# Performance work log

Measured on AMD Instinct MI355X. Metric: run time of the kernel, lower is better.

Reference implementation:

```python
import jax, jax.numpy as jnp
import numpy as np

EMBED_DIM = 128
NUM_HEADS = 16
D_K = EMBED_DIM // NUM_HEADS  # n_wires per head = 8
DEPTH = 1
DIM = 2 ** D_K  # 256 state amplitudes


def _cnot_chain_inverse_perm(d, depth):
    """Inverse permutation of basis states under `depth` rounds of the CNOT ladder
    CNOT(0,1),...,CNOT(d-2,d-1),CNOT(d-1,0). Wire 0 = most significant bit."""
    idx = np.arange(2 ** d)
    shifts = d - 1 - np.arange(d)
    bits = (idx[:, None] >> shifts) & 1  # (2^d, d)
    for _ in range(depth):
        for w in range(d - 1):
            bits[:, w + 1] ^= bits[:, w]
        bits[:, 0] ^= bits[:, d - 1]
    fwd = (bits << shifts).sum(axis=1)  # psi'[fwd[b]] = psi[b]
    inv = np.empty_like(fwd)
    inv[fwd] = idx  # psi'[j] = psi[inv[j]]
    return inv


def _pauliz_signs(d):
    idx = np.arange(2 ** d)
    shifts = d - 1 - np.arange(d)
    bits = (idx[:, None] >> shifts) & 1
    return (1.0 - 2.0 * bits).astype(np.float32)  # (2^d, d)


_INV_PERM = jnp.asarray(_cnot_chain_inverse_perm(D_K, DEPTH))
_SIGNS = jnp.asarray(_pauliz_signs(D_K))


def quantum_head(angles):
    """angles: (..., d) RX rotation angles. Returns PauliZ expectations (..., d).

    Product state amplitudes after per-wire RX from |0..0>: probabilities are
    products of cos^2/sin^2; CNOT ladder is a basis permutation; <Z_w> is a
    signed sum of probabilities."""
    half = angles * 0.5
    c2 = jnp.cos(half) ** 2
    s2 = jnp.sin(half) ** 2
    lead = angles.shape[:-1]
    p = jnp.ones(lead + (1,), angles.dtype)
    for w in range(D_K):  # builds (..., 2^d) probability vector
        pair = jnp.stack([c2[..., w], s2[..., w]], axis=-1)
        p = (p[..., :, None] * pair[..., None, :]).reshape(lead + (-1,))
    p = p[..., _INV_PERM]  # apply CNOT ladder permutation
    return p @ _SIGNS  # (..., d) PauliZ expectations


def setup_inputs() -> dict:
    key = jax.random.key(0)
    ks = jax.random.split(key, 10)
    B, S, E = 8, 512, EMBED_DIM
    sc = 1.0 / np.sqrt(E)
    return {
        "x": jax.random.normal(ks[0], (B, S, E), jnp.float32),
        "Wq": jax.random.normal(ks[1], (E, E), jnp.float32) * sc,
        "bq": jnp.zeros((E,), jnp.float32),
        "Wk": jax.random.normal(ks[2], (E, E), jnp.float32) * sc,
        "bk": jnp.zeros((E,), jnp.float32),
        "Wv": jax.random.normal(ks[3], (E, E), jnp.float32) * sc,
        "bv": jnp.zeros((E,), jnp.float32),
        "Wo": jax.random.normal(ks[4], (E, E), jnp.float32) * sc,
        "bo": jnp.zeros((E,), jnp.float32),
        "theta": jax.random.normal(ks[5], (NUM_HEADS, D_K), jnp.float32),
    }


def reference(x, Wq, bq, Wk, bk, Wv, bv, Wo, bo, theta):
    B, S, E = x.shape
    H, dk = NUM_HEADS, D_K

    def split_heads(y):  # (B,S,E) -> (B,H,S,dk)
        return y.reshape(B, S, H, dk).transpose(0, 2, 1, 3)

    q = split_heads(x @ Wq + bq)
    k = split_heads(x @ Wk + bk)
    v = split_heads(x @ Wv + bv)

    th = theta[None, :, None, :]  # broadcast per-head trainable RX angles
    qh = quantum_head(q + th)
    kh = quantum_head(k + th)
    vh = quantum_head(v + th)

    scores = jnp.einsum("bhsd,bhtd->bhst", qh, kh) / jnp.sqrt(jnp.asarray(dk, x.dtype))
    attn = jax.nn.softmax(scores, axis=-1)
    out = jnp.einsum("bhst,bhtd->bhsd", attn, vh)
    out = out.transpose(0, 2, 1, 3).reshape(B, S, E)
    return out @ Wo + bo
```

## Files before the change

### kernel.cpp

```cpp
#include <hip/hip_runtime.h>
#include <hip/hip_bf16.h>
#include <math.h>

#define BB 8
#define SS 512
#define EE 128
#define HH 16
#define DKK 8

#define FMA4(ACC, S, W) do { (ACC).x += (S)*(W).x; (ACC).y += (S)*(W).y; \
                             (ACC).z += (S)*(W).z; (ACC).w += (S)*(W).w; } while(0)
#define ADD4(A, B) do { (A).x += (B).x; (A).y += (B).y; (A).z += (B).z; (A).w += (B).w; } while(0)
#define DOT4(A, B) ((A).x*(B).x + (A).y*(B).y + (A).z*(B).z + (A).w*(B).w)

__global__ __launch_bounds__(256, 4) void k_qkvq(
    const float* __restrict__ x,
    const float* __restrict__ Wq, const float* __restrict__ bq,
    const float* __restrict__ Wk, const float* __restrict__ bk,
    const float* __restrict__ Wv, const float* __restrict__ bv,
    const float* __restrict__ theta,
    float* __restrict__ qh, float* __restrict__ kh, float* __restrict__ vh)
{
    __shared__ float xs[16][128];
    const int t = threadIdx.x;
    const int m = blockIdx.y;
    const int row0 = blockIdx.x * 16;

    {
        const float4* xv = (const float4*)(x + (size_t)row0 * 128);
        float4* xsv = (float4*)&xs[0][0];
        xsv[t]       = xv[t];
        xsv[t + 256] = xv[t + 256];
    }
    __syncthreads();

    const int cg   = t & 31;
    const int col0 = cg * 4;
    const int rg   = t >> 5;
    const int r0   = rg * 2;

    const float* __restrict__ W  = (m == 0) ? Wq : (m == 1) ? Wk : Wv;
    const float* __restrict__ bb = (m == 0) ? bq : (m == 1) ? bk : bv;
    float* __restrict__ outp     = (m == 0) ? qh : (m == 1) ? kh : vh;

    float4 acc0 = *(const float4*)&bb[col0];
    float4 acc1 = acc0;

    #pragma unroll 4
    for (int k4 = 0; k4 < 32; ++k4) {
        const float4 xa = ((const float4*)xs[r0 + 0])[k4];
        const float4 xb = ((const float4*)xs[r0 + 1])[k4];
        const float4 w0 = *(const float4*)&W[(k4 * 4 + 0) * 128 + col0];
        const float4 w1 = *(const float4*)&W[(k4 * 4 + 1) * 128 + col0];
        const float4 w2 = *(const float4*)&W[(k4 * 4 + 2) * 128 + col0];
        const float4 w3 = *(const float4*)&W[(k4 * 4 + 3) * 128 + col0];
        FMA4(acc0, xa.x, w0); FMA4(acc0, xa.y, w1);
        FMA4(acc0, xa.z, w2); FMA4(acc0, xa.w, w3);
        FMA4(acc1, xb.x, w0); FMA4(acc1, xb.y, w1);
        FMA4(acc1, xb.z, w2); FMA4(acc1, xb.w, w3);
    }

    const float4 th = *(const float4*)&theta[col0];
    const int h    = cg >> 1;
    const int half = cg & 1;

    float4 accs[2] = {acc0, acc1};
    #pragma unroll
    for (int r = 0; r < 2; ++r) {
        float4 c;
        c.x = __cosf(accs[r].x + th.x);
        c.y = __cosf(accs[r].y + th.y);
        c.z = __cosf(accs[r].z + th.z);
        c.w = __cosf(accs[r].w + th.w);
        const float p0 = c.x;
        const float p1 = p0 * c.y;
        const float p2 = p1 * c.z;
        const float p3 = p2 * c.w;
        const float recv = __shfl_xor(p3, 1);
        float4 o;
        if (half == 0) {
            o.x = c.y * c.z * c.w * recv;
            o.y = p1; o.z = p2; o.w = p3;
        } else {
            o.x = recv * p0;
            o.y = recv * p1;
            o.z = recv * p2;
            o.w = recv * p3;
        }
        const int g  = row0 + r0 + r;
        const int b_ = g >> 9;
        const int s  = g & 511;
        *(float4*)&outp[(((size_t)b_ * HH + h) * SS + s) * DKK + half * 4] = o;
    }
}

__global__ __launch_bounds__(512, 2) void k_attn(
    const float* __restrict__ qh, const float* __restrict__ kh,
    const float* __restrict__ vh, float* __restrict__ hid)
{
    __shared__ float4 smem[3072];

    const int t  = threadIdx.x;
    const int L  = t & 63;
    const int wv = t >> 6;
    const int bh = blockIdx.x & 127;
    const int q0 = (blockIdx.x >> 7) * 256;

    {
        const float4* kg = (const float4*)kh + (size_t)bh * 1024;
        const float4* vg = (const float4*)vh + (size_t)bh * 1024;
        smem[t]        = kg[t];
        smem[t + 512]  = kg[t + 512];
        smem[1024 + t] = vg[t];
        smem[1536 + t] = vg[t + 512];
    }

    const float sc = 0.51012091944f;
    float4 qa[4], qb[4];
    {
        const float4* qg = (const float4*)qh + ((size_t)bh * 512 + q0) * 2;
        #pragma unroll
        for (int r = 0; r < 4; ++r) {
            float4 a = qg[(L + 64 * r) * 2];
            float4 b = qg[(L + 64 * r) * 2 + 1];
            a.x *= sc; a.y *= sc; a.z *= sc; a.w *= sc;
            b.x *= sc; b.y *= sc; b.z *= sc; b.w *= sc;
            qa[r] = a; qb[r] = b;
        }
    }
    __syncthreads();

    float4 aA[4], aB[4];
    float  den[4];
    #pragma unroll
    for (int r = 0; r < 4; ++r) {
        aA[r] = make_float4(0.f, 0.f, 0.f, 0.f);
        aB[r] = make_float4(0.f, 0.f, 0.f, 0.f);
        den[r] = 0.f;
    }

    const float4* kbase = smem + wv * 128;
    const float4* vbase = smem + 1024 + wv * 128;

    #pragma unroll 4
    for (int j = 0; j < 64; ++j) {
        const float4 k0 = kbase[2 * j];
        const float4 k1 = kbase[2 * j + 1];
        const float4 v0 = vbase[2 * j];
        const float4 v1 = vbase[2 * j + 1];
        #pragma unroll
        for (int r = 0; r < 4; ++r) {
            const float s = DOT4(qa[r], k0) + DOT4(qb[r], k1);
            const float e = exp2f(s);
            den[r] += e;
            FMA4(aA[r], e, v0);
            FMA4(aB[r], e, v1);
        }
    }
    __syncthreads();

    if (wv < 4) {
        #pragma unroll
        for (int r = 0; r < 4; ++r) {
            const int idx = (wv * 256 + L + 64 * r) * 3;
            smem[idx]     = aA[r];
            smem[idx + 1] = aB[r];
            smem[idx + 2] = make_float4(den[r], 0.f, 0.f, 0.f);
        }
    }
    __syncthreads();
    if (wv >= 4) {
        #pragma unroll
        for (int r = 0; r < 4; ++r) {
            const int idx = ((wv - 4) * 256 + L + 64 * r) * 3;
            float4 pa = smem[idx];
            float4 pb = smem[idx + 1];
            float4 pd = smem[idx + 2];
            ADD4(pa, aA[r]); ADD4(pb, aB[r]); pd.x += den[r];
            smem[idx]     = pa;
            smem[idx + 1] = pb;
            smem[idx + 2] = pd;
        }
    }
    __syncthreads();

    if (t < 256) {
        float4 rA = make_float4(0.f, 0.f, 0.f, 0.f), rB = rA;
        float rd = 0.f;
        #pragma unroll
        for (int s4 = 0; s4 < 4; ++s4) {
            const int idx = (s4 * 256 + t) * 3;
            const float4 a = smem[idx];
            const float4 b = smem[idx + 1];
            ADD4(rA, a); ADD4(rB, b);
            rd += smem[idx + 2].x;
        }
        const float inv = 1.0f / rd;
        rA.x *= inv; rA.y *= inv; rA.z *= inv; rA.w *= inv;
        rB.x *= inv; rB.y *= inv; rB.z *= inv; rB.w *= inv;
        const int b_ = bh >> 4, h = bh & 15;
        float* o = hid + ((size_t)(b_ * 512) + q0 + t) * 128 + h * 8;
        ((float4*)o)[0] = rA;
        ((float4*)o)[1] = rB;
    }
}

__global__ __launch_bounds__(256, 4) void k_out(
    const float* __restrict__ hid, const float* __restrict__ Wo,
    const float* __restrict__ bo, float* __restrict__ out)
{
    __shared__ float hs[16][128];
    const int t = threadIdx.x;
    const int row0 = blockIdx.x * 16;

    {
        const float4* hv = (const float4*)(hid + (size_t)row0 * 128);
        float4* hsv = (float4*)&hs[0][0];
        hsv[t]       = hv[t];
        hsv[t + 256] = hv[t + 256];
    }
    __syncthreads();

    const int cg   = t & 31;
    const int col0 = cg * 4;
    const int rg   = t >> 5;
    const int r0   = rg * 2;

    float4 acc0 = *(const float4*)&bo[col0];
    float4 acc1 = acc0;

    #pragma unroll 4
    for (int k4 = 0; k4 < 32; ++k4) {
        const float4 xa = ((const float4*)hs[r0 + 0])[k4];
        const float4 xb = ((const float4*)hs[r0 + 1])[k4];
        const float4 w0 = *(const float4*)&Wo[(k4 * 4 + 0) * 128 + col0];
        const float4 w1 = *(const float4*)&Wo[(k4 * 4 + 1) * 128 + col0];
        const float4 w2 = *(const float4*)&Wo[(k4 * 4 + 2) * 128 + col0];
        const float4 w3 = *(const float4*)&Wo[(k4 * 4 + 3) * 128 + col0];
        FMA4(acc0, xa.x, w0); FMA4(acc0, xa.y, w1);
        FMA4(acc0, xa.z, w2); FMA4(acc0, xa.w, w3);
        FMA4(acc1, xb.x, w0); FMA4(acc1, xb.y, w1);
        FMA4(acc1, xb.z, w2); FMA4(acc1, xb.w, w3);
    }

    *(float4*)&out[(size_t)(row0 + r0 + 0) * 128 + col0] = acc0;
    *(float4*)&out[(size_t)(row0 + r0 + 1) * 128 + col0] = acc1;
}

extern "C" void kernel_launch(void* const* d_in, const int* in_sizes, int n_in,
                              void* d_out, int out_size, void* d_ws, size_t ws_size,
                              hipStream_t stream)
{
    const float* x     = (const float*)d_in[0];
    const float* Wq    = (const float*)d_in[1];
    const float* bq    = (const float*)d_in[2];
    const float* Wk    = (const float*)d_in[3];
    const float* bk    = (const float*)d_in[4];
    const float* Wv    = (const float*)d_in[5];
    const float* bv    = (const float*)d_in[6];
    const float* Wo    = (const float*)d_in[7];
    const float* bo    = (const float*)d_in[8];
    const float* theta = (const float*)d_in[9];
    float* out = (float*)d_out;

    float* ws  = (float*)d_ws;
    float* qh  = ws;
    float* kh  = ws + 524288;
    float* vh  = ws + 1048576;
    float* hid = ws + 1572864;

    k_qkvq<<<dim3(256, 3), 256, 0, stream>>>(x, Wq, bq, Wk, bk, Wv, bv,
                                             theta, qh, kh, vh);
    k_attn<<<256, 512, 0, stream>>>(qh, kh, vh, hid);
    k_out <<<256, 256, 0, stream>>>(hid, Wo, bo, out);
}
```

Before: 47.76 us.

## Fuse output projection into attention kernel via per-head atomic accumulation

Drops the separate output-projection kernel and the hid workspace round trip. Each attention block now multiplies its per-head 8-wide result by the matching 8 rows of Wo and atomically adds its contribution into the output, which the QKV kernel pre-initialises with the bias. This saves one kernel launch and a global write and read of hid. In exchange it issues many float atomics (16 heads add into each output element), and the summation order becomes nondeterministic. It also lowers the QKV kernel's launch-bounds occupancy hint.

```diff
diff --git a/kernel.cpp b/kernel.cpp
--- a/kernel.cpp
+++ b/kernel.cpp
@@ -13,13 +13,14 @@
 #define ADD4(A, B) do { (A).x += (B).x; (A).y += (B).y; (A).z += (B).z; (A).w += (B).w; } while(0)
 #define DOT4(A, B) ((A).x*(B).x + (A).y*(B).y + (A).z*(B).z + (A).w*(B).w)
 
-__global__ __launch_bounds__(256, 4) void k_qkvq(
+__global__ __launch_bounds__(256, 2) void k_qkvq(
     const float* __restrict__ x,
     const float* __restrict__ Wq, const float* __restrict__ bq,
     const float* __restrict__ Wk, const float* __restrict__ bk,
     const float* __restrict__ Wv, const float* __restrict__ bv,
-    const float* __restrict__ theta,
-    float* __restrict__ qh, float* __restrict__ kh, float* __restrict__ vh)
+    const float* __restrict__ theta, const float* __restrict__ bo,
+    float* __restrict__ qh, float* __restrict__ kh, float* __restrict__ vh,
+    float* __restrict__ out)
 {
     __shared__ float xs[16][128];
     const int t = threadIdx.x;
@@ -92,19 +93,28 @@
         const int s  = g & 511;
         *(float4*)&outp[(((size_t)b_ * HH + h) * SS + s) * DKK + half * 4] = o;
     }
+
+    if (m == 0) {
+        const float4 b0 = *(const float4*)&bo[col0];
+        *(float4*)&out[(size_t)(row0 + r0 + 0) * 128 + col0] = b0;
+        *(float4*)&out[(size_t)(row0 + r0 + 1) * 128 + col0] = b0;
+    }
 }
 
-__global__ __launch_bounds__(512, 2) void k_attn(
+__global__ __launch_bounds__(512, 2) void k_attn_out(
     const float* __restrict__ qh, const float* __restrict__ kh,
-    const float* __restrict__ vh, float* __restrict__ hid)
+    const float* __restrict__ vh, const float* __restrict__ Wo,
+    float* __restrict__ out)
 {
-    __shared__ float4 smem[3072];
+    __shared__ float4 smem[3584];
 
     const int t  = threadIdx.x;
     const int L  = t & 63;
     const int wv = t >> 6;
     const int bh = blockIdx.x & 127;
     const int q0 = (blockIdx.x >> 7) * 256;
+    const int b_ = bh >> 4;
+    const int h  = bh & 15;
 
     {
         const float4* kg = (const float4*)kh + (size_t)bh * 1024;
@@ -198,53 +208,30 @@
         const float inv = 1.0f / rd;
         rA.x *= inv; rA.y *= inv; rA.z *= inv; rA.w *= inv;
         rB.x *= inv; rB.y *= inv; rB.z *= inv; rB.w *= inv;
-        const int b_ = bh >> 4, h = bh & 15;
-        float* o = hid + ((size_t)(b_ * 512) + q0 + t) * 128 + h * 8;
-        ((float4*)o)[0] = rA;
-        ((float4*)o)[1] = rB;
-    }
-}
-
-__global__ __launch_bounds__(256, 4) void k_out(
-    const float* __restrict__ hid, const float* __restrict__ Wo,
-    const float* __restrict__ bo, float* __restrict__ out)
-{
-    __shared__ float hs[16][128];
-    const int t = threadIdx.x;
-    const int row0 = blockIdx.x * 16;
-
-    {
-        const float4* hv = (const float4*)(hid + (size_t)row0 * 128);
-        float4* hsv = (float4*)&hs[0][0];
-        hsv[t]       = hv[t];
-        hsv[t + 256] = hv[t + 256];
-    }
-    __syncthreads();
-
-    const int cg   = t & 31;
-    const int col0 = cg * 4;
-    const int rg   = t >> 5;
-    const int r0   = rg * 2;
-
-    float4 acc0 = *(const float4*)&bo[col0];
-    float4 acc1 = acc0;
-
-    #pragma unroll 4
-    for (int k4 = 0; k4 < 32; ++k4) {
-        const float4 xa = ((const float4*)hs[r0 + 0])[k4];
-        const float4 xb = ((const float4*)hs[r0 + 1])[k4];
-        const float4 w0 = *(const float4*)&Wo[(k4 * 4 + 0) * 128 + col0];
-        const float4 w1 = *(const float4*)&Wo[(k4 * 4 + 1) * 128 + col0];
-        const float4 w2 = *(const float4*)&Wo[(k4 * 4 + 2) * 128 + col0];
-        const float4 w3 = *(const float4*)&Wo[(k4 * 4 + 3) * 128 + col0];
-        FMA4(acc0, xa.x, w0); FMA4(acc0, xa.y, w1);
-        FMA4(acc0, xa.z, w2); FMA4(acc0, xa.w, w3);
-        FMA4(acc1, xb.x, w0); FMA4(acc1, xb.y, w1);
-        FMA4(acc1, xb.z, w2); FMA4(acc1, xb.w, w3);
-    }
-
-    *(float4*)&out[(size_t)(row0 + r0 + 0) * 128 + col0] = acc0;
-    *(float4*)&out[(size_t)(row0 + r0 + 1) * 128 + col0] = acc1;
+        smem[3072 + t * 2]     = rA;
+        smem[3072 + t * 2 + 1] = rB;
+    }
+    __syncthreads();
+
+    {
+        const int col = t & 127;
+        const int rg  = t >> 7;
+        float wo[8];
+        #pragma unroll
+        for (int i = 0; i < 8; ++i)
+            wo[i] = Wo[(h * 8 + i) * 128 + col];
+
+        const float* red = (const float*)(smem + 3072);
+        float* obase = out + ((size_t)(b_ * 512) + q0 + rg * 64) * 128 + col;
+        #pragma unroll 4
+        for (int rr = 0; rr < 64; ++rr) {
+            const float4 r0v = *(const float4*)&red[(rg * 64 + rr) * 8];
+            const float4 r1v = *(const float4*)&red[(rg * 64 + rr) * 8 + 4];
+            const float acc = r0v.x*wo[0] + r0v.y*wo[1] + r0v.z*wo[2] + r0v.w*wo[3]
+                            + r1v.x*wo[4] + r1v.y*wo[5] + r1v.z*wo[6] + r1v.w*wo[7];
+            unsafeAtomicAdd(obase + (size_t)rr * 128, acc);
+        }
+    }
 }
 
 extern "C" void kernel_launch(void* const* d_in, const int* in_sizes, int n_in,
@@ -263,14 +250,12 @@
     const float* theta = (const float*)d_in[9];
     float* out = (float*)d_out;
 
-    float* ws  = (float*)d_ws;
-    float* qh  = ws;
-    float* kh  = ws + 524288;
-    float* vh  = ws + 1048576;
-    float* hid = ws + 1572864;
+    float* ws = (float*)d_ws;
+    float* qh = ws;
+    float* kh = ws + 524288;
+    float* vh = ws + 1048576;
 
     k_qkvq<<<dim3(256, 3), 256, 0, stream>>>(x, Wq, bq, Wk, bk, Wv, bv,
-                                             theta, qh, kh, vh);
-    k_attn<<<256, 512, 0, stream>>>(qh, kh, vh, hid);
-    k_out <<<256, 256, 0, stream>>>(hid, Wo, bo, out);
+                                             theta, bo, qh, kh, vh, out);
+    k_attn_out<<<256, 512, 0, stream>>>(qh, kh, vh, Wo, out);
 }
```

Result: slower. 74.00 us (+54.9%).

## Split each wave's key range across half-waves with 8 query rows per lane

Applied to the files above, without the earlier changes.

Each wave previously walked its 64 keys with every lane holding 4 query rows. Now the two half-waves each take half of the wave's keys while every lane holds 8 query rows, and the halves are combined with cross-lane shuffles before the existing shared-memory reduction. This halves LDS reads of K/V per unit of work and exposes more independent exp/FMA chains, at the cost of roughly double the accumulator registers. The occupancy hint in launch bounds is dropped accordingly.

```diff
diff --git a/kernel.cpp b/kernel.cpp
--- a/kernel.cpp
+++ b/kernel.cpp
@@ -94,7 +94,7 @@
     }
 }
 
-__global__ __launch_bounds__(512, 2) void k_attn(
+__global__ __launch_bounds__(512) void k_attn(
     const float* __restrict__ qh, const float* __restrict__ kh,
     const float* __restrict__ vh, float* __restrict__ hid)
 {
@@ -103,6 +103,8 @@
     const int t  = threadIdx.x;
     const int L  = t & 63;
     const int wv = t >> 6;
+    const int hw = L >> 5;
+    const int l5 = L & 31;
     const int bh = blockIdx.x & 127;
     const int q0 = (blockIdx.x >> 7) * 256;
 
@@ -116,13 +118,13 @@
     }
 
     const float sc = 0.51012091944f;
-    float4 qa[4], qb[4];
+    float4 qa[8], qb[8];
     {
         const float4* qg = (const float4*)qh + ((size_t)bh * 512 + q0) * 2;
         #pragma unroll
-        for (int r = 0; r < 4; ++r) {
-            float4 a = qg[(L + 64 * r) * 2];
-            float4 b = qg[(L + 64 * r) * 2 + 1];
+        for (int r = 0; r < 8; ++r) {
+            float4 a = qg[(l5 + 32 * r) * 2];
+            float4 b = qg[(l5 + 32 * r) * 2 + 1];
             a.x *= sc; a.y *= sc; a.z *= sc; a.w *= sc;
             b.x *= sc; b.y *= sc; b.z *= sc; b.w *= sc;
             qa[r] = a; qb[r] = b;
@@ -130,26 +132,26 @@
     }
     __syncthreads();
 
-    float4 aA[4], aB[4];
-    float  den[4];
+    float4 aA[8], aB[8];
+    float  den[8];
     #pragma unroll
-    for (int r = 0; r < 4; ++r) {
+    for (int r = 0; r < 8; ++r) {
         aA[r] = make_float4(0.f, 0.f, 0.f, 0.f);
         aB[r] = make_float4(0.f, 0.f, 0.f, 0.f);
         den[r] = 0.f;
     }
 
-    const float4* kbase = smem + wv * 128;
-    const float4* vbase = smem + 1024 + wv * 128;
+    const float4* kbase = smem + wv * 128 + hw * 64;
+    const float4* vbase = smem + 1024 + wv * 128 + hw * 64;
 
     #pragma unroll 4
-    for (int j = 0; j < 64; ++j) {
-        const float4 k0 = kbase[2 * j];
-        const float4 k1 = kbase[2 * j + 1];
-        const float4 v0 = vbase[2 * j];
-        const float4 v1 = vbase[2 * j + 1];
-        #pragma unroll
-        for (int r = 0; r < 4; ++r) {
+    for (int jj = 0; jj < 32; ++jj) {
+        const float4 k0 = kbase[2 * jj];
+        const float4 k1 = kbase[2 * jj + 1];
+        const float4 v0 = vbase[2 * jj];
+        const float4 v1 = vbase[2 * jj + 1];
+        #pragma unroll
+        for (int r = 0; r < 8; ++r) {
             const float s = DOT4(qa[r], k0) + DOT4(qb[r], k1);
             const float e = exp2f(s);
             den[r] += e;
@@ -157,12 +159,23 @@
             FMA4(aB[r], e, v1);
         }
     }
+
+    #pragma unroll
+    for (int r = 0; r < 8; ++r) {
+        aA[r].x += __shfl_xor(aA[r].x, 32); aA[r].y += __shfl_xor(aA[r].y, 32);
+        aA[r].z += __shfl_xor(aA[r].z, 32); aA[r].w += __shfl_xor(aA[r].w, 32);
+        aB[r].x += __shfl_xor(aB[r].x, 32); aB[r].y += __shfl_xor(aB[r].y, 32);
+        aB[r].z += __shfl_xor(aB[r].z, 32); aB[r].w += __shfl_xor(aB[r].w, 32);
+        den[r]  += __shfl_xor(den[r], 32);
+    }
     __syncthreads();
 
     if (wv < 4) {
         #pragma unroll
-        for (int r = 0; r < 4; ++r) {
-            const int idx = (wv * 256 + L + 64 * r) * 3;
+        for (int rr = 0; rr < 4; ++rr) {
+            const int r   = hw * 4 + rr;
+            const int row = l5 + 32 * r;
+            const int idx = (wv * 256 + row) * 3;
             smem[idx]     = aA[r];
             smem[idx + 1] = aB[r];
             smem[idx + 2] = make_float4(den[r], 0.f, 0.f, 0.f);
@@ -171,8 +184,10 @@
     __syncthreads();
     if (wv >= 4) {
         #pragma unroll
-        for (int r = 0; r < 4; ++r) {
-            const int idx = ((wv - 4) * 256 + L + 64 * r) * 3;
+        for (int rr = 0; rr < 4; ++rr) {
+            const int r   = hw * 4 + rr;
+            const int row = l5 + 32 * r;
+            const int idx = ((wv - 4) * 256 + row) * 3;
             float4 pa = smem[idx];
             float4 pb = smem[idx + 1];
             float4 pd = smem[idx + 2];
```

New measurement: 57.49 us. 20.4% more time.
